# Optimization experiments

Hardware: AMD Instinct MI355X
Metric: run time of the kernel (lower is better)

The kernel has to match this reference:

```python
import jax, jax.numpy as jnp
import numpy as np

B = 8192
N_IN = 16 * 12 * 64  # 12288
H0, H1, H2 = 256, 32, 32
OUTPUT_SCALE = 300.0
WDL_SCALE = 200.0


def setup_inputs() -> dict:
    key = jax.random.key(0)
    ks = jax.random.split(key, 12)
    # In real NNUE these are ~30-hot binary vectors; math is identical for dense rand.
    white_features = (jax.random.uniform(ks[0], (B, N_IN)) < 0.0025).astype(jnp.float32)
    black_features = (jax.random.uniform(ks[1], (B, N_IN)) < 0.0025).astype(jnp.float32)
    side = jax.random.randint(ks[2], (B,), 0, 2).astype(bool)
    ft_std = np.sqrt(2.0 / (22 + H1))
    ft_w = jax.random.normal(ks[3], (H0, N_IN)) * ft_std
    ft_b = jnp.zeros((H0,))
    def xavier(k, fan_out, fan_in):
        std = np.sqrt(2.0 / (fan_in + fan_out))
        return jax.random.normal(k, (fan_out, fan_in)) * std
    l1_w = xavier(ks[4], H1, 2 * H0)
    l1_b = jnp.zeros((H1,))
    l2_w = xavier(ks[5], H2, H1)
    l2_b = jnp.zeros((H2,))
    l3_w = xavier(ks[6], 1, H2)
    l3_b = jnp.zeros((1,))
    return {"white_features": white_features, "black_features": black_features,
            "side": side, "ft_w": ft_w, "ft_b": ft_b, "l1_w": l1_w, "l1_b": l1_b,
            "l2_w": l2_w, "l2_b": l2_b, "l3_w": l3_w, "l3_b": l3_b}


def reference(white_features, black_features, side, ft_w, ft_b,
              l1_w, l1_b, l2_w, l2_b, l3_w, l3_b):
    w = white_features @ ft_w.T + ft_b  # [B, H0]
    b = black_features @ ft_w.T + ft_b  # [B, H0]
    s = side[:, None]  # [B, 1] bool
    # side-to-move first: white -> [w, b], black -> [b, w]
    acc = jnp.where(s, jnp.concatenate([w, b], axis=1),
                    jnp.concatenate([b, w], axis=1))  # [B, 2*H0]
    o0 = jnp.clip(acc, 0.0, 1.0)
    o1 = jnp.clip(o0 @ l1_w.T + l1_b, 0.0, 1.0)
    o2 = jnp.clip(o1 @ l2_w.T + l2_b, 0.0, 1.0)
    o3 = (o2 @ l3_w.T + l3_b) * OUTPUT_SCALE  # [B, 1]
    return jax.nn.sigmoid(o3 / WDL_SCALE)
```

## Files before the change

### kernel.cpp

```cpp
#include <hip/hip_runtime.h>
#include <math.h>


#define NIN   12288
#define NF4   3072
#define FPT   12
#define H0    256
#define MAXF  192

__global__ __launch_bounds__(256) void transpose_ftw(const float* __restrict__ src,
                                                     float* __restrict__ dst) {
    __shared__ float tile[32][33];
    const int jb = blockIdx.x * 32;
    const int hb = blockIdx.y * 32;
    const int tx = threadIdx.x;
    const int ty = threadIdx.y;
#pragma unroll
    for (int r = 0; r < 32; r += 8)
        tile[ty + r][tx] = src[(size_t)(hb + ty + r) * NIN + jb + tx];
    __syncthreads();
#pragma unroll
    for (int r = 0; r < 32; r += 8)
        dst[(size_t)(jb + ty + r) * H0 + hb + tx] = tile[tx][ty + r];
}

template <bool TRANSPOSED>
__global__ __launch_bounds__(256) void nnue_kernel(
    const float* __restrict__ white,
    const float* __restrict__ black,
    const int* __restrict__ side,
    const float* __restrict__ ftw,
    const float* __restrict__ ft_b,
    const float* __restrict__ l1_w,
    const float* __restrict__ l1_b,
    const float* __restrict__ l2_w,
    const float* __restrict__ l2_b,
    const float* __restrict__ l3_w,
    const float* __restrict__ l3_b,
    float* __restrict__ out)
{
    __shared__ int w_list[MAXF];
    __shared__ int b_list[MAXF];
    __shared__ int w_cnt, b_cnt;
    __shared__ float sh_o0[512] __attribute__((aligned(16)));
    __shared__ float sh_o1[32];
    __shared__ float sh_o2[32];

    const int s   = blockIdx.x;
    const int tid = threadIdx.x;

    if (tid == 0) { w_cnt = 0; b_cnt = 0; }
    __syncthreads();

    const uint4* wrow = (const uint4*)(white + (size_t)s * NIN);
    const uint4* brow = (const uint4*)(black + (size_t)s * NIN);
#pragma unroll
    for (int i = 0; i < FPT; ++i) {
        const int v = i * 256 + tid;
        uint4 u = wrow[v];
        if (u.x | u.y | u.z | u.w) {
            if (u.x) { int p = atomicAdd(&w_cnt, 1); if (p < MAXF) w_list[p] = v * 4 + 0; }
            if (u.y) { int p = atomicAdd(&w_cnt, 1); if (p < MAXF) w_list[p] = v * 4 + 1; }
            if (u.z) { int p = atomicAdd(&w_cnt, 1); if (p < MAXF) w_list[p] = v * 4 + 2; }
            if (u.w) { int p = atomicAdd(&w_cnt, 1); if (p < MAXF) w_list[p] = v * 4 + 3; }
        }
        uint4 ub = brow[v];
        if (ub.x | ub.y | ub.z | ub.w) {
            if (ub.x) { int p = atomicAdd(&b_cnt, 1); if (p < MAXF) b_list[p] = v * 4 + 0; }
            if (ub.y) { int p = atomicAdd(&b_cnt, 1); if (p < MAXF) b_list[p] = v * 4 + 1; }
            if (ub.z) { int p = atomicAdd(&b_cnt, 1); if (p < MAXF) b_list[p] = v * 4 + 2; }
            if (ub.w) { int p = atomicAdd(&b_cnt, 1); if (p < MAXF) b_list[p] = v * 4 + 3; }
        }
    }
    __syncthreads();

    const int wn = min(w_cnt, MAXF);
    const int bn = min(b_cnt, MAXF);

    const float bias = ft_b[tid];
    float wacc = bias;
    float bacc = bias;
    for (int k = 0; k < wn; ++k) {
        const int j = w_list[k];
        wacc += TRANSPOSED ? ftw[(size_t)j * H0 + tid] : ftw[(size_t)tid * NIN + j];
    }
    for (int k = 0; k < bn; ++k) {
        const int j = b_list[k];
        bacc += TRANSPOSED ? ftw[(size_t)j * H0 + tid] : ftw[(size_t)tid * NIN + j];
    }
    const float ow = fminf(fmaxf(wacc, 0.f), 1.f);
    const float ob = fminf(fmaxf(bacc, 0.f), 1.f);
    const bool sd = (side[s] != 0);
    sh_o0[tid]       = sd ? ow : ob;
    sh_o0[256 + tid] = sd ? ob : ow;
    __syncthreads();

    {
        const int o = tid >> 3;
        const int p = tid & 7;
        const float4* wp = (const float4*)(l1_w + (o * 512 + p * 64));
        const float4* xp = (const float4*)(sh_o0 + p * 64);
        float sum = 0.f;
#pragma unroll
        for (int v = 0; v < 16; ++v) {
            float4 w4 = wp[v];
            float4 x4 = xp[v];
            sum += w4.x * x4.x + w4.y * x4.y + w4.z * x4.z + w4.w * x4.w;
        }
        sum += __shfl_down(sum, 4, 8);
        sum += __shfl_down(sum, 2, 8);
        sum += __shfl_down(sum, 1, 8);
        if (p == 0) sh_o1[o] = fminf(fmaxf(sum + l1_b[o], 0.f), 1.f);
    }
    __syncthreads();

    if (tid < 32) {
        float sum = 0.f;
#pragma unroll
        for (int k = 0; k < 32; ++k) sum += l2_w[tid * 32 + k] * sh_o1[k];
        sh_o2[tid] = fminf(fmaxf(sum + l2_b[tid], 0.f), 1.f);
    }
    __syncthreads();

    if (tid < 32) {
        float p = l3_w[tid] * sh_o2[tid];
        p += __shfl_down(p, 16, 32);
        p += __shfl_down(p, 8, 32);
        p += __shfl_down(p, 4, 32);
        p += __shfl_down(p, 2, 32);
        p += __shfl_down(p, 1, 32);
        if (tid == 0) {
            const float o3  = (p + l3_b[0]) * 300.0f;
            const float sig = 1.0f / (1.0f + expf(-o3 / 200.0f));
            out[s] = sig;
        }
    }
}

extern "C" void kernel_launch(void* const* d_in, const int* in_sizes, int n_in,
                              void* d_out, int out_size, void* d_ws, size_t ws_size,
                              hipStream_t stream) {
    const float* white = (const float*)d_in[0];
    const float* black = (const float*)d_in[1];
    const int*   side  = (const int*)d_in[2];
    const float* ft_w  = (const float*)d_in[3];
    const float* ft_b  = (const float*)d_in[4];
    const float* l1_w  = (const float*)d_in[5];
    const float* l1_b  = (const float*)d_in[6];
    const float* l2_w  = (const float*)d_in[7];
    const float* l2_b  = (const float*)d_in[8];
    const float* l3_w  = (const float*)d_in[9];
    const float* l3_b  = (const float*)d_in[10];
    float*       out   = (float*)d_out;

    const int B = in_sizes[2];
    const size_t t_bytes = (size_t)NIN * H0 * sizeof(float);

    if (ws_size >= t_bytes) {
        float* ftw_t = (float*)d_ws;
        hipLaunchKernelGGL(transpose_ftw, dim3(NIN / 32, H0 / 32), dim3(32, 8), 0, stream,
                           ft_w, ftw_t);
        hipLaunchKernelGGL((nnue_kernel<true>), dim3(B), dim3(256), 0, stream,
                           white, black, side, ftw_t, ft_b, l1_w, l1_b, l2_w, l2_b, l3_w, l3_b, out);
    } else {
        hipLaunchKernelGGL((nnue_kernel<false>), dim3(B), dim3(256), 0, stream,
                           white, black, side, ft_w, ft_b, l1_w, l1_b, l2_w, l2_b, l3_w, l3_b, out);
    }
}
```

Before: 840.9 us.

## Split feature scan into grid-stride kernel with global index lists

Moves sparse feature detection out of the per-sample block into a separate grid-stride scan kernel. It writes per-sample index lists and counts to workspace using global atomics, and a gather kernel then consumes them. The aim is better memory-level parallelism on the large dense input reads, plus more outstanding loads in the gather via an 8-way unroll. It adds extra launches, workspace traffic, global atomic contention, and nondeterministic summation order. The L1 loop is also rotated per lane to spread shared-memory accesses.

New measurement: 913.6 us. 8.6% more time.

```diff
diff --git a/kernel.cpp b/kernel.cpp
--- a/kernel.cpp
+++ b/kernel.cpp
@@ -24,10 +24,61 @@
         dst[(size_t)(jb + ty + r) * H0 + hb + tx] = tile[tx][ty + r];
 }
 
-template <bool TRANSPOSED>
-__global__ __launch_bounds__(256) void nnue_kernel(
-    const float* __restrict__ white,
-    const float* __restrict__ black,
+__global__ __launch_bounds__(256) void zero_counts(int* __restrict__ cnts, int n) {
+    const int i = blockIdx.x * 256 + threadIdx.x;
+    if (i < n) cnts[i] = 0;
+}
+
+__device__ __forceinline__ void scanv(uint4 u, int i,
+                                      int* __restrict__ cnts,
+                                      int* __restrict__ lists) {
+    if (u.x | u.y | u.z | u.w) {
+        const int s  = i / NF4;
+        const int jb = (i - s * NF4) << 2;
+        int* lst = lists + (size_t)s * MAXF;
+        int* c   = cnts + s;
+        if (u.x) { int p = atomicAdd(c, 1); if (p < MAXF) lst[p] = jb + 0; }
+        if (u.y) { int p = atomicAdd(c, 1); if (p < MAXF) lst[p] = jb + 1; }
+        if (u.z) { int p = atomicAdd(c, 1); if (p < MAXF) lst[p] = jb + 2; }
+        if (u.w) { int p = atomicAdd(c, 1); if (p < MAXF) lst[p] = jb + 3; }
+    }
+}
+
+__global__ __launch_bounds__(256) void scan_kernel(const uint4* __restrict__ white,
+                                                   const uint4* __restrict__ black,
+                                                   int* __restrict__ cnts,
+                                                   int* __restrict__ lists,
+                                                   int total)
+{
+    const int stride = gridDim.x * 256;
+    int i = blockIdx.x * 256 + threadIdx.x;
+    int* cnts_b  = cnts;
+    const int B = total / NF4;
+    for (; i + 3 * stride < total; i += 4 * stride) {
+        const uint4 w0 = white[i];
+        const uint4 w1 = white[i + stride];
+        const uint4 w2 = white[i + 2 * stride];
+        const uint4 w3 = white[i + 3 * stride];
+        const uint4 b0 = black[i];
+        const uint4 b1 = black[i + stride];
+        const uint4 b2 = black[i + 2 * stride];
+        const uint4 b3 = black[i + 3 * stride];
+        scanv(w0, i,              cnts_b, lists);
+        scanv(w1, i + stride,     cnts_b, lists);
+        scanv(w2, i + 2 * stride, cnts_b, lists);
+        scanv(w3, i + 3 * stride, cnts_b, lists);
+        scanv(b0, i + B * NF4,              cnts_b, lists);
+        scanv(b1, i + stride + B * NF4,     cnts_b, lists);
+        scanv(b2, i + 2 * stride + B * NF4, cnts_b, lists);
+        scanv(b3, i + 3 * stride + B * NF4, cnts_b, lists);
+    }
+    for (; i < total; i += stride) {
+        scanv(white[i], i, cnts_b, lists);
+        scanv(black[i], i + B * NF4, cnts_b, lists);
+    }
+}
+
+__global__ __launch_bounds__(256) void gather_kernel(
     const int* __restrict__ side,
     const float* __restrict__ ftw,
     const float* __restrict__ ft_b,
@@ -37,11 +88,13 @@
     const float* __restrict__ l2_b,
     const float* __restrict__ l3_w,
     const float* __restrict__ l3_b,
-    float* __restrict__ out)
+    const int* __restrict__ cnts,
+    const int* __restrict__ lists,
+    float* __restrict__ out,
+    int B)
 {
     __shared__ int w_list[MAXF];
     __shared__ int b_list[MAXF];
-    __shared__ int w_cnt, b_cnt;
     __shared__ float sh_o0[512] __attribute__((aligned(16)));
     __shared__ float sh_o1[32];
     __shared__ float sh_o2[32];
@@ -49,44 +102,43 @@
     const int s   = blockIdx.x;
     const int tid = threadIdx.x;
 
-    if (tid == 0) { w_cnt = 0; b_cnt = 0; }
-    __syncthreads();
-
-    const uint4* wrow = (const uint4*)(white + (size_t)s * NIN);
-    const uint4* brow = (const uint4*)(black + (size_t)s * NIN);
-#pragma unroll
-    for (int i = 0; i < FPT; ++i) {
-        const int v = i * 256 + tid;
-        uint4 u = wrow[v];
-        if (u.x | u.y | u.z | u.w) {
-            if (u.x) { int p = atomicAdd(&w_cnt, 1); if (p < MAXF) w_list[p] = v * 4 + 0; }
-            if (u.y) { int p = atomicAdd(&w_cnt, 1); if (p < MAXF) w_list[p] = v * 4 + 1; }
-            if (u.z) { int p = atomicAdd(&w_cnt, 1); if (p < MAXF) w_list[p] = v * 4 + 2; }
-            if (u.w) { int p = atomicAdd(&w_cnt, 1); if (p < MAXF) w_list[p] = v * 4 + 3; }
-        }
-        uint4 ub = brow[v];
-        if (ub.x | ub.y | ub.z | ub.w) {
-            if (ub.x) { int p = atomicAdd(&b_cnt, 1); if (p < MAXF) b_list[p] = v * 4 + 0; }
-            if (ub.y) { int p = atomicAdd(&b_cnt, 1); if (p < MAXF) b_list[p] = v * 4 + 1; }
-            if (ub.z) { int p = atomicAdd(&b_cnt, 1); if (p < MAXF) b_list[p] = v * 4 + 2; }
-            if (ub.w) { int p = atomicAdd(&b_cnt, 1); if (p < MAXF) b_list[p] = v * 4 + 3; }
-        }
-    }
-    __syncthreads();
-
-    const int wn = min(w_cnt, MAXF);
-    const int bn = min(b_cnt, MAXF);
+    const int wn = min(cnts[s], MAXF);
+    const int bn = min(cnts[B + s], MAXF);
+    if (tid < wn) w_list[tid] = lists[(size_t)s * MAXF + tid];
+    if (tid < bn) b_list[tid] = lists[(size_t)(B + s) * MAXF + tid];
+    __syncthreads();
 
     const float bias = ft_b[tid];
+    const float* col = ftw + tid;
     float wacc = bias;
     float bacc = bias;
-    for (int k = 0; k < wn; ++k) {
-        const int j = w_list[k];
-        wacc += TRANSPOSED ? ftw[(size_t)j * H0 + tid] : ftw[(size_t)tid * NIN + j];
-    }
-    for (int k = 0; k < bn; ++k) {
-        const int j = b_list[k];
-        bacc += TRANSPOSED ? ftw[(size_t)j * H0 + tid] : ftw[(size_t)tid * NIN + j];
+    {
+        int k = 0;
+        for (; k + 8 <= wn; k += 8) {
+            const float f0 = col[(size_t)w_list[k]     * H0];
+            const float f1 = col[(size_t)w_list[k + 1] * H0];
+            const float f2 = col[(size_t)w_list[k + 2] * H0];
+            const float f3 = col[(size_t)w_list[k + 3] * H0];
+            const float f4 = col[(size_t)w_list[k + 4] * H0];
+            const float f5 = col[(size_t)w_list[k + 5] * H0];
+            const float f6 = col[(size_t)w_list[k + 6] * H0];
+            const float f7 = col[(size_t)w_list[k + 7] * H0];
+            wacc += ((f0 + f1) + (f2 + f3)) + ((f4 + f5) + (f6 + f7));
+        }
+        for (; k < wn; ++k) wacc += col[(size_t)w_list[k] * H0];
+        k = 0;
+        for (; k + 8 <= bn; k += 8) {
+            const float f0 = col[(size_t)b_list[k]     * H0];
+            const float f1 = col[(size_t)b_list[k + 1] * H0];
+            const float f2 = col[(size_t)b_list[k + 2] * H0];
+            const float f3 = col[(size_t)b_list[k + 3] * H0];
+            const float f4 = col[(size_t)b_list[k + 4] * H0];
+            const float f5 = col[(size_t)b_list[k + 5] * H0];
+            const float f6 = col[(size_t)b_list[k + 6] * H0];
+            const float f7 = col[(size_t)b_list[k + 7] * H0];
+            bacc += ((f0 + f1) + (f2 + f3)) + ((f4 + f5) + (f6 + f7));
+        }
+        for (; k < bn; ++k) bacc += col[(size_t)b_list[k] * H0];
     }
     const float ow = fminf(fmaxf(wacc, 0.f), 1.f);
     const float ob = fminf(fmaxf(bacc, 0.f), 1.f);
@@ -102,7 +154,8 @@
         const float4* xp = (const float4*)(sh_o0 + p * 64);
         float sum = 0.f;
 #pragma unroll
-        for (int v = 0; v < 16; ++v) {
+        for (int i = 0; i < 16; ++i) {
+            const int v = (2 * p + i) & 15;
             float4 w4 = wp[v];
             float4 x4 = xp[v];
             sum += w4.x * x4.x + w4.y * x4.y + w4.z * x4.z + w4.w * x4.w;
@@ -133,6 +186,100 @@
             const float o3  = (p + l3_b[0]) * 300.0f;
             const float sig = 1.0f / (1.0f + expf(-o3 / 200.0f));
             out[s] = sig;
+        }
+    }
+}
+
+template <bool TRANSPOSED>
+__global__ __launch_bounds__(256) void nnue_kernel(
+    const float* __restrict__ white, const float* __restrict__ black,
+    const int* __restrict__ side, const float* __restrict__ ftw,
+    const float* __restrict__ ft_b, const float* __restrict__ l1_w,
+    const float* __restrict__ l1_b, const float* __restrict__ l2_w,
+    const float* __restrict__ l2_b, const float* __restrict__ l3_w,
+    const float* __restrict__ l3_b, float* __restrict__ out)
+{
+    __shared__ int w_list[MAXF];
+    __shared__ int b_list[MAXF];
+    __shared__ int w_cnt, b_cnt;
+    __shared__ float sh_o0[512] __attribute__((aligned(16)));
+    __shared__ float sh_o1[32];
+    __shared__ float sh_o2[32];
+    const int s = blockIdx.x, tid = threadIdx.x;
+    if (tid == 0) { w_cnt = 0; b_cnt = 0; }
+    __syncthreads();
+    const uint4* wrow = (const uint4*)(white + (size_t)s * NIN);
+    const uint4* brow = (const uint4*)(black + (size_t)s * NIN);
+#pragma unroll
+    for (int i = 0; i < FPT; ++i) {
+        const int v = i * 256 + tid;
+        uint4 u = wrow[v];
+        if (u.x | u.y | u.z | u.w) {
+            if (u.x) { int p = atomicAdd(&w_cnt, 1); if (p < MAXF) w_list[p] = v * 4 + 0; }
+            if (u.y) { int p = atomicAdd(&w_cnt, 1); if (p < MAXF) w_list[p] = v * 4 + 1; }
+            if (u.z) { int p = atomicAdd(&w_cnt, 1); if (p < MAXF) w_list[p] = v * 4 + 2; }
+            if (u.w) { int p = atomicAdd(&w_cnt, 1); if (p < MAXF) w_list[p] = v * 4 + 3; }
+        }
+        uint4 b = brow[v];
+        if (b.x | b.y | b.z | b.w) {
+            if (b.x) { int p = atomicAdd(&b_cnt, 1); if (p < MAXF) b_list[p] = v * 4 + 0; }
+            if (b.y) { int p = atomicAdd(&b_cnt, 1); if (p < MAXF) b_list[p] = v * 4 + 1; }
+            if (b.z) { int p = atomicAdd(&b_cnt, 1); if (p < MAXF) b_list[p] = v * 4 + 2; }
+            if (b.w) { int p = atomicAdd(&b_cnt, 1); if (p < MAXF) b_list[p] = v * 4 + 3; }
+        }
+    }
+    __syncthreads();
+    const int wn = min(w_cnt, MAXF), bn = min(b_cnt, MAXF);
+    const float bias = ft_b[tid];
+    float wacc = bias, bacc = bias;
+    for (int k = 0; k < wn; ++k) {
+        const int j = w_list[k];
+        wacc += TRANSPOSED ? ftw[(size_t)j * H0 + tid] : ftw[(size_t)tid * NIN + j];
+    }
+    for (int k = 0; k < bn; ++k) {
+        const int j = b_list[k];
+        bacc += TRANSPOSED ? ftw[(size_t)j * H0 + tid] : ftw[(size_t)tid * NIN + j];
+    }
+    const float ow = fminf(fmaxf(wacc, 0.f), 1.f);
+    const float ob = fminf(fmaxf(bacc, 0.f), 1.f);
+    const bool sd = (side[s] != 0);
+    sh_o0[tid] = sd ? ow : ob;
+    sh_o0[256 + tid] = sd ? ob : ow;
+    __syncthreads();
+    {
+        const int o = tid >> 3, p = tid & 7;
+        const float4* wp = (const float4*)(l1_w + (o * 512 + p * 64));
+        const float4* xp = (const float4*)(sh_o0 + p * 64);
+        float sum = 0.f;
+#pragma unroll
+        for (int i = 0; i < 16; ++i) {
+            const int v = (2 * p + i) & 15;
+            float4 w4 = wp[v]; float4 x4 = xp[v];
+            sum += w4.x * x4.x + w4.y * x4.y + w4.z * x4.z + w4.w * x4.w;
+        }
+        sum += __shfl_down(sum, 4, 8);
+        sum += __shfl_down(sum, 2, 8);
+        sum += __shfl_down(sum, 1, 8);
+        if (p == 0) sh_o1[o] = fminf(fmaxf(sum + l1_b[o], 0.f), 1.f);
+    }
+    __syncthreads();
+    if (tid < 32) {
+        float sum = 0.f;
+#pragma unroll
+        for (int k = 0; k < 32; ++k) sum += l2_w[tid * 32 + k] * sh_o1[k];
+        sh_o2[tid] = fminf(fmaxf(sum + l2_b[tid], 0.f), 1.f);
+    }
+    __syncthreads();
+    if (tid < 32) {
+        float p = l3_w[tid] * sh_o2[tid];
+        p += __shfl_down(p, 16, 32);
+        p += __shfl_down(p, 8, 32);
+        p += __shfl_down(p, 4, 32);
+        p += __shfl_down(p, 2, 32);
+        p += __shfl_down(p, 1, 32);
+        if (tid == 0) {
+            const float o3 = (p + l3_b[0]) * 300.0f;
+            out[s] = 1.0f / (1.0f + expf(-o3 / 200.0f));
         }
     }
 }
@@ -154,9 +301,27 @@
     float*       out   = (float*)d_out;
 
     const int B = in_sizes[2];
-    const size_t t_bytes = (size_t)NIN * H0 * sizeof(float);
-
-    if (ws_size >= t_bytes) {
+    const size_t t_floats   = (size_t)NIN * H0;
+    const size_t cnt_ints   = (size_t)2 * B;
+    const size_t list_ints  = (size_t)2 * B * MAXF;
+    const size_t need_bytes = t_floats * 4 + (cnt_ints + list_ints) * 4;
+
+    if (ws_size >= need_bytes) {
+        float* ftw_t = (float*)d_ws;
+        int*   cnts  = (int*)((char*)d_ws + t_floats * 4);
+        int*   lists = cnts + cnt_ints;
+        const int total = B * NF4;
+
+        hipLaunchKernelGGL(zero_counts, dim3((int)((cnt_ints + 255) / 256)), dim3(256),
+                           0, stream, cnts, (int)cnt_ints);
+        hipLaunchKernelGGL(transpose_ftw, dim3(NIN / 32, H0 / 32), dim3(32, 8), 0, stream,
+                           ft_w, ftw_t);
+        hipLaunchKernelGGL(scan_kernel, dim3(2048), dim3(256), 0, stream,
+                           (const uint4*)white, (const uint4*)black, cnts, lists, total);
+        hipLaunchKernelGGL(gather_kernel, dim3(B), dim3(256), 0, stream,
+                           side, ftw_t, ft_b, l1_w, l1_b, l2_w, l2_b, l3_w, l3_b,
+                           cnts, lists, out, B);
+    } else if (ws_size >= t_floats * 4) {
         float* ftw_t = (float*)d_ws;
         hipLaunchKernelGGL(transpose_ftw, dim3(NIN / 32, H0 / 32), dim3(32, 8), 0, stream,
                            ft_w, ftw_t);
```
